# Kernel optimization log

Hardware: AMD Instinct MI355X
Metric: run time of the kernel (lower is better)

The kernel has to match this reference:

```python
import jax, jax.numpy as jnp
import numpy as np

N = 100000   # nodes
E = 1600000  # edges (before self-loops)
H = 4        # heads
C = 16       # out channels per head
NEG_SLOPE = 0.2


def _gat_layer(x, src, dst, W, a_src, a_dst, b):
    # x: [N, Fin]; W: [Fin, H*C]; a_src/a_dst: [H, C]; b: [H*C]
    h = (x @ W).reshape(N, H, C)                       # [N, H, C]
    e_s = jnp.einsum('nhc,hc->nh', h, a_src)           # [N, H]
    e_d = jnp.einsum('nhc,hc->nh', h, a_dst)           # [N, H]
    e = e_s[src] + e_d[dst]                            # [E', H]
    e = jax.nn.leaky_relu(e, NEG_SLOPE)
    # segment softmax over destination nodes
    m = jax.ops.segment_max(e, dst, num_segments=N)    # [N, H]
    ex = jnp.exp(e - m[dst])
    s = jax.ops.segment_sum(ex, dst, num_segments=N)   # [N, H]
    alpha = ex / (s[dst] + 1e-16)                      # [E', H]
    msg = alpha[:, :, None] * h[src]                   # [E', H, C]
    out = jax.ops.segment_sum(msg, dst, num_segments=N)  # [N, H, C]
    return out.reshape(N, H * C) + b


def setup_inputs() -> dict:
    key = jax.random.key(0)
    ks = jax.random.split(key, 24)
    g = lambda k, shp, sc=0.1: (jax.random.normal(k, shp, jnp.float32) * sc)
    inp = {
        'x': jax.random.normal(ks[0], (N, 1), jnp.float32),
        'edge_index': jax.random.randint(ks[1], (2, E), 0, N, dtype=jnp.int32),
        # GAT layer 0: in=1
        'W0': g(ks[2], (1, H * C)), 'as0': g(ks[3], (H, C)), 'ad0': g(ks[4], (H, C)), 'b0': jnp.zeros((H * C,), jnp.float32),
        # GAT layer 1: in=64
        'W1': g(ks[5], (H * C, H * C)), 'as1': g(ks[6], (H, C)), 'ad1': g(ks[7], (H, C)), 'b1': jnp.zeros((H * C,), jnp.float32),
        # GAT layer 2: in=64
        'W2': g(ks[8], (H * C, H * C)), 'as2': g(ks[9], (H, C)), 'ad2': g(ks[10], (H, C)), 'b2': jnp.zeros((H * C,), jnp.float32),
        # latent MLP: Linear(64,64) -> ReLU -> Linear(64,16)
        'lw1': g(ks[11], (H * C, 64)), 'lb1': jnp.zeros((64,), jnp.float32),
        'lw2': g(ks[12], (64, 16)), 'lb2': jnp.zeros((16,), jnp.float32),
        # decoder: Linear(16,4) -> Softmax
        'dw': g(ks[13], (16, 4)), 'db': jnp.zeros((4,), jnp.float32),
    }
    return inp


def reference(x, edge_index, W0, as0, ad0, b0, W1, as1, ad1, b1, W2, as2, ad2, b2, lw1, lb1, lw2, lb2, dw, db):
    # add self-loops (PyG GATConv default add_self_loops=True)
    loops = jnp.arange(N, dtype=edge_index.dtype)
    src = jnp.concatenate([edge_index[0], loops])
    dst = jnp.concatenate([edge_index[1], loops])
    h = _gat_layer(x, src, dst, W0, as0, ad0, b0)
    h = _gat_layer(h, src, dst, W1, as1, ad1, b1)
    h = _gat_layer(h, src, dst, W2, as2, ad2, b2)
    h = jax.nn.relu(h @ lw1 + lb1)
    h = h @ lw2 + lb2
    logits = h @ dw + db
    return jax.nn.softmax(logits, axis=-1)
```

## Files before the change

### kernel.cpp

```cpp
#include <hip/hip_runtime.h>
#include <hip/hip_fp16.h>
#include <math.h>

#define NN 100000
#define EE 1600000
#define EP (EE + NN)
#define NEG 0.2f
#define TN 128
#define BW 256
#define NB 391
#define CHUNK 4096
#define SSTRIDE 5120
#define SCAP 5120

typedef __attribute__((ext_vector_type(2))) float floatx2;

__device__ inline unsigned pk_fp8x4(float a, float b, float c, float d) {
    unsigned r = __builtin_amdgcn_cvt_pk_fp8_f32(a, b, 0u, false);
    r = __builtin_amdgcn_cvt_pk_fp8_f32(c, d, r, true);
    return r;
}

__device__ __forceinline__ void accum_fp8p(uint2 raw, float p, floatx2* acc) {
    floatx2 p2; p2[0] = p; p2[1] = p;
    acc[0] += p2 * __builtin_amdgcn_cvt_pk_f32_fp8(raw.x, false);
    acc[1] += p2 * __builtin_amdgcn_cvt_pk_f32_fp8(raw.x, true);
    acc[2] += p2 * __builtin_amdgcn_cvt_pk_f32_fp8(raw.y, false);
    acc[3] += p2 * __builtin_amdgcn_cvt_pk_f32_fp8(raw.y, true);
}

__device__ __forceinline__ int wave_iscan(int v, int lane) {
#pragma unroll
    for (int o = 1; o < 64; o <<= 1) {
        int t = __shfl_up(v, o);
        if (lane >= o) v += t;
    }
    return v;
}


__global__ __launch_bounds__(512) void partition_k(const int* __restrict__ ei, int* __restrict__ gcur,
                                                   unsigned int* __restrict__ arena) {
    __shared__ int lh[512], lcur[512], lbase[512];
    __shared__ int wsum[8];
    __shared__ unsigned int staged[CHUNK];
    __shared__ unsigned short stb[CHUNK];
    int tid = threadIdx.x;
    int lane = tid & 63, wid = tid >> 6;
    int c0 = blockIdx.x * CHUNK;
    int csize = min(CHUNK, EP - c0);
    lh[tid] = 0;
    __syncthreads();
    unsigned int myv[8];
    int myb[8];
#pragma unroll
    for (int i = 0; i < 8; i++) {
        int e = c0 + i * 512 + tid;
        if (e < c0 + csize) {
            int d = (e < EE) ? ei[EE + e] : (e - EE);
            int sv = (e < EE) ? ei[e] : d;
            int b = d >> 8;
            myv[i] = ((unsigned)(d - (b << 8)) << 17) | (unsigned)sv;
            myb[i] = b;
            atomicAdd(&lh[b], 1);
        } else myb[i] = -1;
    }
    __syncthreads();
    int v = lh[tid];
    int isc = wave_iscan(v, lane);
    if (lane == 63) wsum[wid] = isc;
    __syncthreads();
    if (tid == 0) {
        int run = 0;
#pragma unroll
        for (int w = 0; w < 8; w++) { int t = wsum[w]; wsum[w] = run; run += t; }
    }
    __syncthreads();
    int excl = isc - v + wsum[wid];
    lcur[tid] = excl;
    __syncthreads();
#pragma unroll
    for (int i = 0; i < 8; i++) {
        if (myb[i] >= 0) {
            int idx = atomicAdd(&lcur[myb[i]], 1);
            staged[idx] = myv[i];
            stb[idx] = (unsigned short)myb[i];
        }
    }
    __syncthreads();
    if (tid < NB && v > 0) {
        int base = atomicAdd(&gcur[tid], v);
        lbase[tid] = tid * SSTRIDE + base - excl;
    }
    __syncthreads();
    for (int i = tid; i < csize; i += 512) {
        unsigned int val = staged[i];
        arena[lbase[stb[i]] + i] = val;
    }
}

__global__ __launch_bounds__(512) void bscan_k(const int* __restrict__ gcur, int* __restrict__ bbase,
                                               int* __restrict__ rowptr) {
    __shared__ int s[512];
    int tid = threadIdx.x;
    int v = (tid < NB) ? gcur[tid] : 0;
    s[tid] = v;
    __syncthreads();
    for (int o = 1; o < 512; o <<= 1) {
        int t = (tid >= o) ? s[tid - o] : 0;
        __syncthreads();
        s[tid] += t;
        __syncthreads();
    }
    int excl = s[tid] - v;
    if (tid <= NB) bbase[tid] = excl;
    if (tid == 0) rowptr[NN] = EP;
}


__global__ __launch_bounds__(512) void csr_scatter_k(const int* __restrict__ bbase, const int* __restrict__ gcur,
                                                     const unsigned int* __restrict__ arena,
                                                     int* __restrict__ rowptr, int* __restrict__ edge_src) {
    __shared__ int cnt[256], sc[256];
    __shared__ int wsum[4];
    __shared__ unsigned int stg[SCAP];
    __shared__ int pos[SCAP];
    __shared__ unsigned short rk[SCAP];
    int tid = threadIdx.x;
    int b = blockIdx.x;
    int e0 = bbase[b];
    int sz = min(gcur[b], SCAP);
    int abase = b * SSTRIDE;
    if (tid < 256) cnt[tid] = 0;
    __syncthreads();
    for (int i = tid; i < sz; i += 512) {
        unsigned int v = arena[abase + i];
        stg[i] = v;
        rk[i] = (unsigned short)atomicAdd(&cnt[v >> 17], 1);
    }
    __syncthreads();
    if (tid < 256) {
        int lane = tid & 63, wid = tid >> 6;
        int v = cnt[tid];
        int isc = wave_iscan(v, lane);
        if (lane == 63) wsum[wid] = isc;
        __syncthreads();
        if (tid == 0) {
            int run = 0;
#pragma unroll
            for (int w = 0; w < 4; w++) { int t = wsum[w]; wsum[w] = run; run += t; }
        }
        __syncthreads();
        int excl = isc - v + wsum[wid];
        int d = (b << 8) + tid;
        if (d < NN) rowptr[d] = e0 + excl;
        sc[tid] = excl;
    } else {
        __syncthreads();
        __syncthreads();
    }
    __syncthreads();
    for (int i = tid; i < sz; i += 512) {
        unsigned int val = stg[i];
        int p = sc[val >> 17] + rk[i];
        pos[p] = (int)(val & 0x1FFFFu);
    }
    __syncthreads();
    for (int i = tid; i < sz; i += 512) {
        edge_src[e0 + i] = pos[i];
    }
}


__global__ __launch_bounds__(256) void gather0_k(const float* __restrict__ x, const float* __restrict__ W0,
                                                 const float* __restrict__ as_, const float* __restrict__ ad_,
                                                 const int* __restrict__ rowptr, const int* __restrict__ edge_src,
                                                 const float* __restrict__ b, __half* __restrict__ hout) {
    __shared__ float W0l[64], asl[64], adl[64], bl[64];
    int tid = threadIdx.x;
    if (tid < 64) { W0l[tid] = W0[tid]; asl[tid] = as_[tid]; adl[tid] = ad_[tid]; bl[tid] = b[tid]; }
    __syncthreads();
    int wv = (blockIdx.x * 256 + tid) >> 6;
    int lane = tid & 63;
    if (wv >= NN) return;
    int q = lane >> 2, head = lane & 3;
    float cs = 0.f, cd = 0.f;
#pragma unroll
    for (int c = 0; c < 16; c++) {
        float w = W0l[head * 16 + c];
        cs += w * asl[head * 16 + c];
        cd += w * adl[head * 16 + c];
    }
    int beg = rowptr[wv], end = rowptr[wv + 1];
    float xd = x[wv];
    float num = 0.f, den = 0.f;
    for (int e0 = beg; e0 < end; e0 += 16) {
        int e = e0 + q;
        bool vld = e < end;
        int ee = vld ? e : (end - 1);
        int src = edge_src[ee];
        float xs = x[src];
        float ev = xs * cs + xd * cd;
        ev = ev > 0.f ? ev : NEG * ev;
        float p = vld ? __expf(ev) : 0.f;
        num += p * xs;
        den += p;
    }
    num += __shfl_xor(num, 4);  num += __shfl_xor(num, 8);
    num += __shfl_xor(num, 16); num += __shfl_xor(num, 32);
    den += __shfl_xor(den, 4);  den += __shfl_xor(den, 8);
    den += __shfl_xor(den, 16); den += __shfl_xor(den, 32);
    float nh = __shfl(num, lane >> 4);
    float dh = __shfl(den, lane >> 4);
    float val = nh / (dh + 1e-16f);
    float hv = val * W0l[lane] + bl[lane];
    hout[((size_t)wv << 6) + lane] = __float2half(hv);
}


__global__ __launch_bounds__(256) void transform64_k(const __half* __restrict__ hin, const float* __restrict__ W,
                                                     const float* __restrict__ as_, const float* __restrict__ ad_,
                                                     unsigned char* __restrict__ h8, float* __restrict__ es, float* __restrict__ ed) {
    __shared__ float At[64 * TN];
    __shared__ float Wl[64 * 64];
    int tid = threadIdx.x;
    for (int i = tid; i < 4096; i += 256) Wl[i] = W[i];
    int n0 = blockIdx.x * TN;
    {
        int row = tid >> 1, hf = tid & 1;
        int n = n0 + row;
        const uint4* src = (const uint4*)(hin + ((size_t)n << 6) + (hf << 5));
#pragma unroll
        for (int i = 0; i < 4; i++) {
            uint4 raw = make_uint4(0, 0, 0, 0);
            if (n < NN) raw = src[i];
            __half2* hh = (__half2*)&raw;
            int c = (hf << 5) + (i << 3);
#pragma unroll
            for (int j = 0; j < 4; j++) {
                float2 f = __half22float2(hh[j]);
                At[(c + 2 * j) * TN + row]     = f.x;
                At[(c + 2 * j + 1) * TN + row] = f.y;
            }
        }
    }
    __syncthreads();
    int c = tid & 15, r = tid >> 4;
    float acc[8][4];
#pragma unroll
    for (int i = 0; i < 8; i++)
#pragma unroll
        for (int j = 0; j < 4; j++) acc[i][j] = 0.f;
#pragma unroll 4
    for (int k = 0; k < 64; k++) {
        float4 a0 = *(float4*)&At[k * TN + r * 8];
        float4 a1 = *(float4*)&At[k * TN + r * 8 + 4];
        float4 w  = *(float4*)&Wl[k * 64 + c * 4];
        float av[8] = {a0.x, a0.y, a0.z, a0.w, a1.x, a1.y, a1.z, a1.w};
#pragma unroll
        for (int i = 0; i < 8; i++) {
            acc[i][0] += av[i] * w.x; acc[i][1] += av[i] * w.y;
            acc[i][2] += av[i] * w.z; acc[i][3] += av[i] * w.w;
        }
    }
    int head = c >> 2, qq = c & 3;
    float as0v = as_[head * 16 + qq * 4], as1v = as_[head * 16 + qq * 4 + 1];
    float as2v = as_[head * 16 + qq * 4 + 2], as3v = as_[head * 16 + qq * 4 + 3];
    float ad0v = ad_[head * 16 + qq * 4], ad1v = ad_[head * 16 + qq * 4 + 1];
    float ad2v = ad_[head * 16 + qq * 4 + 2], ad3v = ad_[head * 16 + qq * 4 + 3];
#pragma unroll
    for (int i = 0; i < 8; i++) {
        int n = n0 + r * 8 + i;
        float pes = acc[i][0] * as0v + acc[i][1] * as1v + acc[i][2] * as2v + acc[i][3] * as3v;
        float ped = acc[i][0] * ad0v + acc[i][1] * ad1v + acc[i][2] * ad2v + acc[i][3] * ad3v;
        pes += __shfl_xor(pes, 1); pes += __shfl_xor(pes, 2);
        ped += __shfl_xor(ped, 1); ped += __shfl_xor(ped, 2);
        if (n < NN) {
            unsigned rq = pk_fp8x4(acc[i][0], acc[i][1], acc[i][2], acc[i][3]);
            *(unsigned*)(h8 + ((size_t)n << 6) + (c << 2)) = rq;
            if (qq == 0) { es[n * 4 + head] = pes; ed[n * 4 + head] = ped; }
        }
    }
}


__global__ __launch_bounds__(256) void gather_k(const unsigned char* __restrict__ h8, const float* __restrict__ es,
                                                const float* __restrict__ ed, const int* __restrict__ rowptr,
                                                const int* __restrict__ edge_src, const float* __restrict__ b,
                                                __half* __restrict__ hout) {
    int pr = (blockIdx.x * 256 + threadIdx.x) >> 6;
    int lane = threadIdx.x & 63;
    int nA = pr * 2;
    if (nA >= NN) return;
    int nB = nA + 1;
    bool hasB = nB < NN;
    int q = lane >> 3, j = lane & 7, head = j >> 1;
    const unsigned char* h8j = h8 + (j << 3);
    int begA = rowptr[nA], endA = rowptr[nA + 1];
    int begB = hasB ? rowptr[nB] : begA, endB = hasB ? rowptr[nB + 1] : begA;
    float edvA = ed[nA * 4 + head];
    float edvB = hasB ? ed[nB * 4 + head] : 0.f;
    floatx2 accA[4], accB[4];
#pragma unroll
    for (int t = 0; t < 4; t++) { accA[t] = (floatx2)(0.f); accB[t] = (floatx2)(0.f); }
    float sA = 0.f, sB = 0.f;
    int iters = max((endA - begA + 7) >> 3, (endB - begB + 7) >> 3);
    for (int k = 0; k < iters; k++) {
        int eA = begA + (k << 3) + q;
        int eB = begB + (k << 3) + q;
        bool vA = eA < endA;
        bool vB = eB < endB;
        int srcA = edge_src[vA ? eA : begA];
        int srcB = edge_src[vB ? eB : begB];
        uint2 rawA = *(const uint2*)(h8j + ((unsigned)srcA << 6));
        float esvA = es[srcA * 4 + head];
        uint2 rawB = *(const uint2*)(h8j + ((unsigned)srcB << 6));
        float esvB = es[srcB * 4 + head];
        float evA = esvA + edvA; evA = evA > 0.f ? evA : NEG * evA;
        float evB = esvB + edvB; evB = evB > 0.f ? evB : NEG * evB;
        float pA = vA ? __expf(evA) : 0.f;
        float pB = vB ? __expf(evB) : 0.f;
        accum_fp8p(rawA, pA, accA);
        accum_fp8p(rawB, pB, accB);
        sA += pA;
        sB += pB;
    }
    float fA[8], fB[8];
#pragma unroll
    for (int t = 0; t < 4; t++) {
        fA[2 * t] = accA[t][0]; fA[2 * t + 1] = accA[t][1];
        fB[2 * t] = accB[t][0]; fB[2 * t + 1] = accB[t][1];
    }
#pragma unroll
    for (int t = 0; t < 8; t++) {
        fA[t] += __shfl_xor(fA[t], 8);
        fA[t] += __shfl_xor(fA[t], 16);
        fA[t] += __shfl_xor(fA[t], 32);
        fB[t] += __shfl_xor(fB[t], 8);
        fB[t] += __shfl_xor(fB[t], 16);
        fB[t] += __shfl_xor(fB[t], 32);
    }
    sA += __shfl_xor(sA, 8); sA += __shfl_xor(sA, 16); sA += __shfl_xor(sA, 32);
    sB += __shfl_xor(sB, 8); sB += __shfl_xor(sB, 16); sB += __shfl_xor(sB, 32);
    if (q == 0) {
        const float4* bp = (const float4*)(b + j * 8);
        float4 b0 = bp[0], b1 = bp[1];
        {
            float inv = 1.0f / (sA + 1e-16f);
            union { __half2 h2[4]; uint4 u; } pk;
            pk.h2[0] = __floats2half2_rn(fA[0] * inv + b0.x, fA[1] * inv + b0.y);
            pk.h2[1] = __floats2half2_rn(fA[2] * inv + b0.z, fA[3] * inv + b0.w);
            pk.h2[2] = __floats2half2_rn(fA[4] * inv + b1.x, fA[5] * inv + b1.y);
            pk.h2[3] = __floats2half2_rn(fA[6] * inv + b1.z, fA[7] * inv + b1.w);
            *(uint4*)(hout + ((size_t)nA << 6) + (j << 3)) = pk.u;
        }
        if (hasB) {
            float inv = 1.0f / (sB + 1e-16f);
            union { __half2 h2[4]; uint4 u; } pk;
            pk.h2[0] = __floats2half2_rn(fB[0] * inv + b0.x, fB[1] * inv + b0.y);
            pk.h2[1] = __floats2half2_rn(fB[2] * inv + b0.z, fB[3] * inv + b0.w);
            pk.h2[2] = __floats2half2_rn(fB[4] * inv + b1.x, fB[5] * inv + b1.y);
            pk.h2[3] = __floats2half2_rn(fB[6] * inv + b1.z, fB[7] * inv + b1.w);
            *(uint4*)(hout + ((size_t)nB << 6) + (j << 3)) = pk.u;
        }
    }
}


__global__ __launch_bounds__(256) void mlp_k(const __half* __restrict__ h, const float* __restrict__ lw1,
                                             const float* __restrict__ lb1, const float* __restrict__ lw2,
                                             const float* __restrict__ lb2, const float* __restrict__ dw,
                                             const float* __restrict__ db, float* __restrict__ out) {
    __shared__ float At[64 * TN];
    __shared__ float W1l[4096];
    __shared__ float W2l[1024];
    __shared__ float dwl[64];
    __shared__ float dbl[4];
    int tid = threadIdx.x;
    for (int i = tid; i < 4096; i += 256) W1l[i] = lw1[i];
    for (int i = tid; i < 1024; i += 256) W2l[i] = lw2[i];
    if (tid < 64) dwl[tid] = dw[tid];
    if (tid < 4) dbl[tid] = db[tid];
    int n0 = blockIdx.x * TN;
    {
        int row = tid >> 1, hf = tid & 1;
        int n = n0 + row;
        const uint4* src = (const uint4*)(h + ((size_t)n << 6) + (hf << 5));
#pragma unroll
        for (int i = 0; i < 4; i++) {
            uint4 raw = make_uint4(0, 0, 0, 0);
            if (n < NN) raw = src[i];
            __half2* hh = (__half2*)&raw;
            int c = (hf << 5) + (i << 3);
#pragma unroll
            for (int j = 0; j < 4; j++) {
                float2 f = __half22float2(hh[j]);
                At[(c + 2 * j) * TN + row]     = f.x;
                At[(c + 2 * j + 1) * TN + row] = f.y;
            }
        }
    }
    __syncthreads();
    int c = tid & 15, r = tid >> 4;
    float acc[8][4];
#pragma unroll
    for (int i = 0; i < 8; i++)
#pragma unroll
        for (int j = 0; j < 4; j++) acc[i][j] = 0.f;
#pragma unroll 4
    for (int k = 0; k < 64; k++) {
        float4 a0 = *(float4*)&At[k * TN + r * 8];
        float4 a1 = *(float4*)&At[k * TN + r * 8 + 4];
        float4 w  = *(float4*)&W1l[k * 64 + c * 4];
        float av[8] = {a0.x, a0.y, a0.z, a0.w, a1.x, a1.y, a1.z, a1.w};
#pragma unroll
        for (int i = 0; i < 8; i++) {
            acc[i][0] += av[i] * w.x; acc[i][1] += av[i] * w.y;
            acc[i][2] += av[i] * w.z; acc[i][3] += av[i] * w.w;
        }
    }
    float b1v0 = lb1[c * 4], b1v1 = lb1[c * 4 + 1], b1v2 = lb1[c * 4 + 2], b1v3 = lb1[c * 4 + 3];
    __syncthreads();
#pragma unroll
    for (int i = 0; i < 8; i++) {
        int n = r * 8 + i;
        At[(c * 4 + 0) * TN + n] = fmaxf(acc[i][0] + b1v0, 0.f);
        At[(c * 4 + 1) * TN + n] = fmaxf(acc[i][1] + b1v1, 0.f);
        At[(c * 4 + 2) * TN + n] = fmaxf(acc[i][2] + b1v2, 0.f);
        At[(c * 4 + 3) * TN + n] = fmaxf(acc[i][3] + b1v3, 0.f);
    }
    __syncthreads();
    float acc2[8];
#pragma unroll
    for (int i = 0; i < 8; i++) acc2[i] = 0.f;
#pragma unroll 4
    for (int k = 0; k < 64; k++) {
        float4 a0 = *(float4*)&At[k * TN + r * 8];
        float4 a1 = *(float4*)&At[k * TN + r * 8 + 4];
        float wv = W2l[k * 16 + c];
        acc2[0] += a0.x * wv; acc2[1] += a0.y * wv; acc2[2] += a0.z * wv; acc2[3] += a0.w * wv;
        acc2[4] += a1.x * wv; acc2[5] += a1.y * wv; acc2[6] += a1.z * wv; acc2[7] += a1.w * wv;
    }
    float b2v = lb2[c];
#pragma unroll
    for (int i = 0; i < 8; i++) W1l[c * TN + r * 8 + i] = acc2[i] + b2v;
    __syncthreads();
    if (tid < TN) {
        int n = n0 + tid;
        if (n < NN) {
            float lg0 = dbl[0], lg1 = dbl[1], lg2 = dbl[2], lg3 = dbl[3];
#pragma unroll
            for (int k = 0; k < 16; k++) {
                float a = W1l[k * TN + tid];
                lg0 += a * dwl[k * 4];     lg1 += a * dwl[k * 4 + 1];
                lg2 += a * dwl[k * 4 + 2]; lg3 += a * dwl[k * 4 + 3];
            }
            float mx = fmaxf(fmaxf(lg0, lg1), fmaxf(lg2, lg3));
            float e0 = __expf(lg0 - mx), e1 = __expf(lg1 - mx), e2 = __expf(lg2 - mx), e3 = __expf(lg3 - mx);
            float inv = 1.0f / (e0 + e1 + e2 + e3);
            *(float4*)(out + (size_t)n * 4) = make_float4(e0 * inv, e1 * inv, e2 * inv, e3 * inv);
        }
    }
}


extern "C" void kernel_launch(void* const* d_in, const int* in_sizes, int n_in,
                              void* d_out, int out_size, void* d_ws, size_t ws_size,
                              hipStream_t stream) {
    const float* x   = (const float*)d_in[0];
    const int*   ei  = (const int*)d_in[1];
    const float* W0  = (const float*)d_in[2];
    const float* as0 = (const float*)d_in[3];
    const float* ad0 = (const float*)d_in[4];
    const float* b0  = (const float*)d_in[5];
    const float* W1  = (const float*)d_in[6];
    const float* as1 = (const float*)d_in[7];
    const float* ad1 = (const float*)d_in[8];
    const float* b1  = (const float*)d_in[9];
    const float* W2  = (const float*)d_in[10];
    const float* as2 = (const float*)d_in[11];
    const float* ad2 = (const float*)d_in[12];
    const float* b2  = (const float*)d_in[13];
    const float* lw1 = (const float*)d_in[14];
    const float* lb1 = (const float*)d_in[15];
    const float* lw2 = (const float*)d_in[16];
    const float* lb2 = (const float*)d_in[17];
    const float* dw  = (const float*)d_in[18];
    const float* db  = (const float*)d_in[19];
    float* out = (float*)d_out;

    char* p = (char*)d_ws;
    size_t off = 0;
    auto alloc = [&](size_t n) -> void* {
        void* r = p + off;
        off = (off + n + 255) & ~(size_t)255;
        return r;
    };
    __half* hB     = (__half*)alloc((size_t)NN * 64 * 2);
    __half* hC     = (__half*)alloc((size_t)NN * 64 * 2);
    unsigned char* h8 = (unsigned char*)alloc((size_t)NN * 64);
    float*  es     = (float*)alloc((size_t)NN * 4 * 4);
    float*  ed     = (float*)alloc((size_t)NN * 4 * 4);
    int*    rowptr = (int*)alloc((size_t)(NN + 1) * 4);
    int*    edge_src = (int*)alloc((size_t)EP * 4);
    unsigned int* arena = (unsigned int*)alloc((size_t)NB * SSTRIDE * 4);
    int*    gcur   = (int*)alloc(512 * 4);
    int*    bbase  = (int*)alloc(513 * 4);

    hipMemsetAsync(gcur, 0, 512 * 4, stream);

    partition_k<<<(EP + CHUNK - 1) / CHUNK, 512, 0, stream>>>(ei, gcur, arena);
    bscan_k<<<1, 512, 0, stream>>>(gcur, bbase, rowptr);
    csr_scatter_k<<<NB, 512, 0, stream>>>(bbase, gcur, arena, rowptr, edge_src);

    int nb_tile = (NN + TN - 1) / TN;
    int nb_wave = (NN + 3) / 4;
    int nb_pair = ((NN + 1) / 2 + 3) / 4;

    gather0_k<<<nb_wave, 256, 0, stream>>>(x, W0, as0, ad0, rowptr, edge_src, b0, hB);

    transform64_k<<<nb_tile, 256, 0, stream>>>(hB, W1, as1, ad1, h8, es, ed);
    gather_k<<<nb_pair, 256, 0, stream>>>(h8, es, ed, rowptr, edge_src, b1, hC);

    transform64_k<<<nb_tile, 256, 0, stream>>>(hC, W2, as2, ad2, h8, es, ed);
    gather_k<<<nb_pair, 256, 0, stream>>>(h8, es, ed, rowptr, edge_src, b2, hB);

    mlp_k<<<nb_tile, 256, 0, stream>>>(hB, lw1, lb1, lw2, lb2, dw, db, out);
}
```

Measured before the change: 306.5 us.

## Fuse layer-0 aggregation and layer-1 transform into CSR scatter kernel

Layer-0 aggregation now runs inside the CSR scatter kernel, reading neighbor lists straight from shared memory, and its output goes directly through the precomposed W0·W1 product to produce layer-1 fp8 features and attention logits. This removes two kernel launches, the fp16 intermediate write and read, and the dense 64x64 transform for layer 1. In exchange the scatter kernel carries more shared memory and a longer serial tail over only 391 blocks, which may limit parallelism for the aggregation work. The algebra relies on layer-0 input being rank-1 per head, so layer-0 output can be written as four per-head scalars.

New measurement: 308.6 us. About the same (+0.7%).

```diff
diff --git a/kernel.cpp b/kernel.cpp
--- a/kernel.cpp
+++ b/kernel.cpp
@@ -120,18 +120,48 @@
 
 __global__ __launch_bounds__(512) void csr_scatter_k(const int* __restrict__ bbase, const int* __restrict__ gcur,
                                                      const unsigned int* __restrict__ arena,
-                                                     int* __restrict__ rowptr, int* __restrict__ edge_src) {
+                                                     int* __restrict__ rowptr, int* __restrict__ edge_src,
+                                                     const float* __restrict__ x, const float* __restrict__ W0,
+                                                     const float* __restrict__ as0, const float* __restrict__ ad0,
+                                                     const float* __restrict__ b0, const float* __restrict__ W1,
+                                                     const float* __restrict__ as1, const float* __restrict__ ad1,
+                                                     unsigned char* __restrict__ h8, float* __restrict__ es,
+                                                     float* __restrict__ ed) {
     __shared__ int cnt[256], sc[256];
     __shared__ int wsum[4];
     __shared__ unsigned int stg[SCAP];
     __shared__ int pos[SCAP];
     __shared__ unsigned short rk[SCAP];
+    __shared__ float G1l[4][64], bb1l[64], asl[64], adl[64], csl[4], cdl[4];
+    __shared__ float vbuf[256][4];
     int tid = threadIdx.x;
     int b = blockIdx.x;
     int e0 = bbase[b];
     int sz = min(gcur[b], SCAP);
     int abase = b * SSTRIDE;
     if (tid < 256) cnt[tid] = 0;
+    if (tid < 64) {
+        float bbv = 0.f;
+#pragma unroll
+        for (int k = 0; k < 64; k++) bbv += b0[k] * W1[k * 64 + tid];
+        bb1l[tid] = bbv;
+#pragma unroll
+        for (int h = 0; h < 4; h++) {
+            float g = 0.f;
+#pragma unroll
+            for (int k = 0; k < 16; k++) g += W0[h * 16 + k] * W1[(h * 16 + k) * 64 + tid];
+            G1l[h][tid] = g;
+        }
+        asl[tid] = as1[tid];
+        adl[tid] = ad1[tid];
+    } else if (tid < 72) {
+        int h = (tid - 64) & 3;
+        float s = 0.f;
+        const float* av = (tid < 68) ? as0 : ad0;
+#pragma unroll
+        for (int c = 0; c < 16; c++) s += W0[h * 16 + c] * av[h * 16 + c];
+        if (tid < 68) csl[h] = s; else cdl[h] = s;
+    }
     __syncthreads();
     for (int i = tid; i < sz; i += 512) {
         unsigned int v = arena[abase + i];
@@ -169,52 +199,64 @@
     for (int i = tid; i < sz; i += 512) {
         edge_src[e0 + i] = pos[i];
     }
-}
-
-
-__global__ __launch_bounds__(256) void gather0_k(const float* __restrict__ x, const float* __restrict__ W0,
-                                                 const float* __restrict__ as_, const float* __restrict__ ad_,
-                                                 const int* __restrict__ rowptr, const int* __restrict__ edge_src,
-                                                 const float* __restrict__ b, __half* __restrict__ hout) {
-    __shared__ float W0l[64], asl[64], adl[64], bl[64];
-    int tid = threadIdx.x;
-    if (tid < 64) { W0l[tid] = W0[tid]; asl[tid] = as_[tid]; adl[tid] = ad_[tid]; bl[tid] = b[tid]; }
-    __syncthreads();
-    int wv = (blockIdx.x * 256 + tid) >> 6;
-    int lane = tid & 63;
-    if (wv >= NN) return;
-    int q = lane >> 2, head = lane & 3;
-    float cs = 0.f, cd = 0.f;
-#pragma unroll
-    for (int c = 0; c < 16; c++) {
-        float w = W0l[head * 16 + c];
-        cs += w * asl[head * 16 + c];
-        cd += w * adl[head * 16 + c];
-    }
-    int beg = rowptr[wv], end = rowptr[wv + 1];
-    float xd = x[wv];
-    float num = 0.f, den = 0.f;
-    for (int e0 = beg; e0 < end; e0 += 16) {
-        int e = e0 + q;
-        bool vld = e < end;
-        int ee = vld ? e : (end - 1);
-        int src = edge_src[ee];
-        float xs = x[src];
-        float ev = xs * cs + xd * cd;
-        ev = ev > 0.f ? ev : NEG * ev;
-        float p = vld ? __expf(ev) : 0.f;
-        num += p * xs;
-        den += p;
-    }
-    num += __shfl_xor(num, 4);  num += __shfl_xor(num, 8);
-    num += __shfl_xor(num, 16); num += __shfl_xor(num, 32);
-    den += __shfl_xor(den, 4);  den += __shfl_xor(den, 8);
-    den += __shfl_xor(den, 16); den += __shfl_xor(den, 32);
-    float nh = __shfl(num, lane >> 4);
-    float dh = __shfl(den, lane >> 4);
-    float val = nh / (dh + 1e-16f);
-    float hv = val * W0l[lane] + bl[lane];
-    hout[((size_t)wv << 6) + lane] = __float2half(hv);
+    {
+        int lane = tid & 63, wid = tid >> 6;
+        int q = lane >> 2, hh = lane & 3;
+        float cs = csl[hh], cd = cdl[hh];
+        for (int dl = wid; dl < 256; dl += 8) {
+            int dg = (b << 8) + dl;
+            if (dg >= NN) break;
+            int beg = sc[dl], len = cnt[dl];
+            float xd = x[dg];
+            float num = 0.f, den = 0.f;
+            for (int k0 = 0; k0 < len; k0 += 16) {
+                int idx = k0 + q;
+                bool vld = idx < len;
+                int src = pos[beg + (vld ? idx : 0)];
+                float xs = x[src];
+                float ev = xs * cs + xd * cd;
+                ev = ev > 0.f ? ev : NEG * ev;
+                float p = vld ? __expf(ev) : 0.f;
+                num += p * xs;
+                den += p;
+            }
+            num += __shfl_xor(num, 4);  num += __shfl_xor(num, 8);
+            num += __shfl_xor(num, 16); num += __shfl_xor(num, 32);
+            den += __shfl_xor(den, 4);  den += __shfl_xor(den, 8);
+            den += __shfl_xor(den, 16); den += __shfl_xor(den, 32);
+            if (q == 0) vbuf[dl][hh] = num / (den + 1e-16f);
+        }
+    }
+    __syncthreads();
+    {
+        int dl = tid >> 1, half = tid & 1;
+        int dg = (b << 8) + dl;
+        if (dg < NN) {
+            float v0 = vbuf[dl][0], v1 = vbuf[dl][1], v2 = vbuf[dl][2], v3 = vbuf[dl][3];
+            float esa0 = 0.f, esa1 = 0.f, eda0 = 0.f, eda1 = 0.f;
+            unsigned pk8[8];
+            int cbase = half << 5;
+#pragma unroll
+            for (int g = 0; g < 8; g++) {
+                float hv[4];
+#pragma unroll
+                for (int u = 0; u < 4; u++) {
+                    int c = cbase + (g << 2) + u;
+                    hv[u] = bb1l[c] + v0 * G1l[0][c] + v1 * G1l[1][c] + v2 * G1l[2][c] + v3 * G1l[3][c];
+                    float e_s = hv[u] * asl[c];
+                    float e_d = hv[u] * adl[c];
+                    if (g < 4) { esa0 += e_s; eda0 += e_d; }
+                    else       { esa1 += e_s; eda1 += e_d; }
+                }
+                pk8[g] = pk_fp8x4(hv[0], hv[1], hv[2], hv[3]);
+            }
+            *(uint4*)(h8 + ((size_t)dg << 6) + (half << 5))      = make_uint4(pk8[0], pk8[1], pk8[2], pk8[3]);
+            *(uint4*)(h8 + ((size_t)dg << 6) + (half << 5) + 16) = make_uint4(pk8[4], pk8[5], pk8[6], pk8[7]);
+            int hb = half << 1;
+            *(float2*)(es + dg * 4 + hb) = make_float2(esa0, esa1);
+            *(float2*)(ed + dg * 4 + hb) = make_float2(eda0, eda1);
+        }
+    }
 }
 
 
@@ -511,15 +553,12 @@
 
     partition_k<<<(EP + CHUNK - 1) / CHUNK, 512, 0, stream>>>(ei, gcur, arena);
     bscan_k<<<1, 512, 0, stream>>>(gcur, bbase, rowptr);
-    csr_scatter_k<<<NB, 512, 0, stream>>>(bbase, gcur, arena, rowptr, edge_src);
+    csr_scatter_k<<<NB, 512, 0, stream>>>(bbase, gcur, arena, rowptr, edge_src,
+                                          x, W0, as0, ad0, b0, W1, as1, ad1, h8, es, ed);
 
     int nb_tile = (NN + TN - 1) / TN;
-    int nb_wave = (NN + 3) / 4;
     int nb_pair = ((NN + 1) / 2 + 3) / 4;
 
-    gather0_k<<<nb_wave, 256, 0, stream>>>(x, W0, as0, ad0, rowptr, edge_src, b0, hB);
-
-    transform64_k<<<nb_tile, 256, 0, stream>>>(hB, W1, as1, ad1, h8, es, ed);
     gather_k<<<nb_pair, 256, 0, stream>>>(h8, es, ed, rowptr, edge_src, b1, hC);
 
     transform64_k<<<nb_tile, 256, 0, stream>>>(hC, W2, as2, ad2, h8, es, ed);
```

## Fuse layer-0 gather with layer-1 transform via precomputed W0·W1 product

Applied to the files above, without the earlier changes.

Layer 0 has input width 1, so its output is a per-head scalar times W0 plus bias. The layer-1 linear map can therefore be folded algebraically into a 4x64 matrix (W0 blocks times W1) plus a bias vector. The gather0 kernel now computes the layer-1 features, fp8-packs them, and produces the attention logits es/ed directly. This removes the transform64 launch and the half-precision round trip of the 64-wide hidden state through memory. In exchange every block redundantly recomputes the small folded matrices in its prologue, using a 64-iteration loop over global W1.

Measured after the change: 321.0 us. 1.05x slower.

```diff
diff --git a/kernel.cpp b/kernel.cpp
--- a/kernel.cpp
+++ b/kernel.cpp
@@ -172,25 +172,43 @@
 }
 
 
-__global__ __launch_bounds__(256) void gather0_k(const float* __restrict__ x, const float* __restrict__ W0,
-                                                 const float* __restrict__ as_, const float* __restrict__ ad_,
-                                                 const int* __restrict__ rowptr, const int* __restrict__ edge_src,
-                                                 const float* __restrict__ b, __half* __restrict__ hout) {
-    __shared__ float W0l[64], asl[64], adl[64], bl[64];
+__global__ __launch_bounds__(256) void g0e_k(const float* __restrict__ x, const float* __restrict__ W0,
+                                             const float* __restrict__ as0, const float* __restrict__ ad0,
+                                             const float* __restrict__ b0, const float* __restrict__ W1,
+                                             const float* __restrict__ as1, const float* __restrict__ ad1,
+                                             const int* __restrict__ rowptr, const int* __restrict__ edge_src,
+                                             unsigned char* __restrict__ h8, float* __restrict__ es,
+                                             float* __restrict__ ed) {
+    __shared__ float G1l[4][64], bb1l[64], asl[64], adl[64], csl[4], cdl[4];
     int tid = threadIdx.x;
-    if (tid < 64) { W0l[tid] = W0[tid]; asl[tid] = as_[tid]; adl[tid] = ad_[tid]; bl[tid] = b[tid]; }
+    if (tid < 64) {
+        float bbv = 0.f;
+#pragma unroll
+        for (int k = 0; k < 64; k++) bbv += b0[k] * W1[k * 64 + tid];
+        bb1l[tid] = bbv;
+#pragma unroll
+        for (int h = 0; h < 4; h++) {
+            float g = 0.f;
+#pragma unroll
+            for (int k = 0; k < 16; k++) g += W0[h * 16 + k] * W1[(h * 16 + k) * 64 + tid];
+            G1l[h][tid] = g;
+        }
+        asl[tid] = as1[tid];
+        adl[tid] = ad1[tid];
+    } else if (tid < 72) {
+        int h = (tid - 64) & 3;
+        float s = 0.f;
+        const float* av = (tid < 68) ? as0 : ad0;
+#pragma unroll
+        for (int c = 0; c < 16; c++) s += W0[h * 16 + c] * av[h * 16 + c];
+        if (tid < 68) csl[h] = s; else cdl[h] = s;
+    }
     __syncthreads();
     int wv = (blockIdx.x * 256 + tid) >> 6;
     int lane = tid & 63;
     if (wv >= NN) return;
     int q = lane >> 2, head = lane & 3;
-    float cs = 0.f, cd = 0.f;
-#pragma unroll
-    for (int c = 0; c < 16; c++) {
-        float w = W0l[head * 16 + c];
-        cs += w * asl[head * 16 + c];
-        cd += w * adl[head * 16 + c];
-    }
+    float cs = csl[head], cd = cdl[head];
     int beg = rowptr[wv], end = rowptr[wv + 1];
     float xd = x[wv];
     float num = 0.f, den = 0.f;
@@ -210,11 +228,25 @@
     num += __shfl_xor(num, 16); num += __shfl_xor(num, 32);
     den += __shfl_xor(den, 4);  den += __shfl_xor(den, 8);
     den += __shfl_xor(den, 16); den += __shfl_xor(den, 32);
-    float nh = __shfl(num, lane >> 4);
-    float dh = __shfl(den, lane >> 4);
-    float val = nh / (dh + 1e-16f);
-    float hv = val * W0l[lane] + bl[lane];
-    hout[((size_t)wv << 6) + lane] = __float2half(hv);
+    float valv = num / (den + 1e-16f);
+    float v0 = __shfl(valv, 0), v1 = __shfl(valv, 1);
+    float v2 = __shfl(valv, 2), v3 = __shfl(valv, 3);
+    float hv = bb1l[lane] + v0 * G1l[0][lane] + v1 * G1l[1][lane]
+             + v2 * G1l[2][lane] + v3 * G1l[3][lane];
+    float h1v = __shfl(hv, lane + 1), h2v = __shfl(hv, lane + 2), h3v = __shfl(hv, lane + 3);
+    if ((lane & 3) == 0) {
+        unsigned rq = pk_fp8x4(hv, h1v, h2v, h3v);
+        *(unsigned*)(h8 + ((size_t)wv << 6) + lane) = rq;
+    }
+    float e_s = hv * asl[lane], e_d = hv * adl[lane];
+    e_s += __shfl_xor(e_s, 1); e_s += __shfl_xor(e_s, 2);
+    e_s += __shfl_xor(e_s, 4); e_s += __shfl_xor(e_s, 8);
+    e_d += __shfl_xor(e_d, 1); e_d += __shfl_xor(e_d, 2);
+    e_d += __shfl_xor(e_d, 4); e_d += __shfl_xor(e_d, 8);
+    if ((lane & 15) == 0) {
+        es[wv * 4 + (lane >> 4)] = e_s;
+        ed[wv * 4 + (lane >> 4)] = e_d;
+    }
 }
 
 
@@ -517,9 +549,9 @@
     int nb_wave = (NN + 3) / 4;
     int nb_pair = ((NN + 1) / 2 + 3) / 4;
 
-    gather0_k<<<nb_wave, 256, 0, stream>>>(x, W0, as0, ad0, rowptr, edge_src, b0, hB);
-
-    transform64_k<<<nb_tile, 256, 0, stream>>>(hB, W1, as1, ad1, h8, es, ed);
+    g0e_k<<<nb_wave, 256, 0, stream>>>(x, W0, as0, ad0, b0, W1, as1, ad1,
+                                       rowptr, edge_src, h8, es, ed);
+
     gather_k<<<nb_pair, 256, 0, stream>>>(h8, es, ed, rowptr, edge_src, b1, hC);
 
     transform64_k<<<nb_tile, 256, 0, stream>>>(hC, W2, as2, ad2, h8, es, ed);
```
